# Kernel tuning notes

Measured on AMD Instinct MI355X. Metric: run time of the kernel, lower is better.

The kernel has to match this reference:

```python
import jax, jax.numpy as jnp
import numpy as np

B, N, D, H, DK = 4, 2048, 1024, 16, 64  # batch, seq, model_dim, heads, key_dim (= value_dim)
NEG = -1e9


def setup_inputs() -> dict:
    key = jax.random.key(0)
    ks = jax.random.split(key, 5)
    X = jax.random.normal(ks[0], (B, N, D), dtype=jnp.float32)
    # causal additive mask [N, N]; module slices mask[:N, :M] and adds to logits
    mask = jnp.where(jnp.tril(jnp.ones((N, N), dtype=bool)), 0.0, NEG).astype(jnp.float32)
    s = 1.0 / np.sqrt(D)
    Wq = jax.random.normal(ks[1], (D, H * DK), dtype=jnp.float32) * s
    Wk = jax.random.normal(ks[2], (D, H * DK), dtype=jnp.float32) * s
    Wv = jax.random.normal(ks[3], (D, H * DK), dtype=jnp.float32) * s
    Wo = jax.random.normal(ks[4], (H * DK, D), dtype=jnp.float32) * s
    return {"X": X, "mask": mask, "Wq": Wq, "Wk": Wk, "Wv": Wv, "Wo": Wo}


def reference(X, mask, Wq, Wk, Wv, Wo):
    # Linear projections (bias=False), then split heads: [B,N,H,DK] -> [B,H,N,DK]
    Q = (X @ Wq).reshape(B, N, H, DK).transpose(0, 2, 1, 3)
    K = (X @ Wk).reshape(B, N, H, DK).transpose(0, 2, 1, 3)
    V = (X @ Wv).reshape(B, N, H, DK).transpose(0, 2, 1, 3)
    # full [B,H,N,N] attention logits (module materializes it explicitly)
    att = jnp.einsum('bhnd,bhmd->bhnm', Q, K) / jnp.sqrt(jnp.float32(DK))
    # dropout is in eval mode here -> identity; then additive mask[:N,:M]
    att = att + mask[:N, :N]
    prob = jax.nn.softmax(att, axis=-1)
    values = jnp.einsum('bhnm,bhmd->bhnd', prob, V)
    values_cat = values.transpose(0, 2, 1, 3).reshape(B, N, H * DK)
    return values_cat @ Wo
```

## Files before the change

### kernel.cpp

```cpp
#include <hip/hip_runtime.h>

typedef _Float16 h4  __attribute__((ext_vector_type(4)));
typedef _Float16 v8h __attribute__((ext_vector_type(8)));
typedef float    v4f __attribute__((ext_vector_type(4)));

constexpr int Bn = 4, Nn = 2048, Dn = 1024, Hn = 16, DKn = 64, Mn = 8192;

__device__ __forceinline__ void load_lds16(const _Float16* g, _Float16* l) {
    __builtin_amdgcn_global_load_lds(
        (const __attribute__((address_space(1))) void*)g,
        (__attribute__((address_space(3))) void*)l, 16, 0, 0);
}

__global__ __launch_bounds__(256) void cast_f16(const float* __restrict__ x,
                                                _Float16* __restrict__ y) {
    const int i = blockIdx.x * 256 + threadIdx.x;
    const float4 v = ((const float4*)x)[i];
    h4 o; o[0] = (_Float16)v.x; o[1] = (_Float16)v.y;
    o[2] = (_Float16)v.z; o[3] = (_Float16)v.w;
    ((h4*)y)[i] = o;
}

__global__ __launch_bounds__(256) void castW4(const float* __restrict__ Wq,
                                              const float* __restrict__ Wk,
                                              const float* __restrict__ Wv,
                                              const float* __restrict__ Wo,
                                              _Float16* __restrict__ Wqkv,
                                              _Float16* __restrict__ Wto) {
    __shared__ float tile[32][33];
    const int which = blockIdx.x >> 10, bid = blockIdx.x & 1023;
    const float* W = which == 0 ? Wq : which == 1 ? Wk : which == 2 ? Wv : Wo;
    _Float16* Dst = which < 3 ? (Wqkv + ((size_t)which << 20)) : Wto;
    const int bx = bid & 31, by = bid >> 5;
    const int t = threadIdx.x;
    const int r = t >> 3, c4 = (t & 7) * 4;
    const float4 v = *(const float4*)&W[(size_t)(by * 32 + r) * Dn + bx * 32 + c4];
    tile[r][c4 + 0] = v.x; tile[r][c4 + 1] = v.y;
    tile[r][c4 + 2] = v.z; tile[r][c4 + 3] = v.w;
    __syncthreads();
    h4 o;
    o[0] = (_Float16)tile[c4 + 0][r];
    o[1] = (_Float16)tile[c4 + 1][r];
    o[2] = (_Float16)tile[c4 + 2][r];
    o[3] = (_Float16)tile[c4 + 3][r];
    *(h4*)&Dst[(size_t)(bx * 32 + r) * Dn + by * 32 + c4] = o;
}

#define GEMM_KLOOP(Abase, Bbase)                                                    \
    v4f acc[4][4];                                                                  \
    _Pragma("unroll") for (int i = 0; i < 4; ++i)                                   \
        _Pragma("unroll") for (int j = 0; j < 4; ++j) acc[i][j] = v4f{0,0,0,0};     \
    const int sw8 = (quad ^ (l16 >> 2)) * 8;                                        \
    for (int k0 = 0; k0 < Dn; k0 += 32) {                                           \
        __syncthreads();                                                            \
        _Pragma("unroll") for (int jj = 0; jj < 2; ++jj) {                          \
            const int ci = jj * 256 + w * 64 + lane;                                \
            const int rs = ci >> 2, cs = ci & 3;                                    \
            const int gc = (cs ^ ((rs >> 2) & 3)) * 8;                              \
            load_lds16(Abase + (size_t)rs * Dn + k0 + gc, &As[(jj*256 + w*64) * 8]);\
            load_lds16(Bbase + (size_t)rs * Dn + k0 + gc, &Bs[(jj*256 + w*64) * 8]);\
        }                                                                           \
        __syncthreads();                                                            \
        v8h a[4], b[4];                                                             \
        _Pragma("unroll") for (int i = 0; i < 4; ++i)                               \
            a[i] = *(const v8h*)&As[(wm*64 + i*16 + l16) * 32 + sw8];               \
        _Pragma("unroll") for (int j = 0; j < 4; ++j)                               \
            b[j] = *(const v8h*)&Bs[(wn*64 + j*16 + l16) * 32 + sw8];               \
        _Pragma("unroll") for (int i = 0; i < 4; ++i)                               \
            _Pragma("unroll") for (int j = 0; j < 4; ++j)                           \
                acc[i][j] = __builtin_amdgcn_mfma_f32_16x16x32_f16(a[i], b[j],      \
                                                                   acc[i][j],0,0,0);\
    }

__global__ __launch_bounds__(256) void gemmqkv(const _Float16* __restrict__ A,
                                               const _Float16* __restrict__ Wt,
                                               _Float16* __restrict__ Qo,
                                               _Float16* __restrict__ Ko,
                                               _Float16* __restrict__ Vo)
{
    __shared__ __align__(16) _Float16 As[128 * 32];
    __shared__ __align__(16) _Float16 Bs[128 * 32];
    const int t = threadIdx.x, lane = t & 63, w = t >> 6;
    const int quad = lane >> 4, l16 = lane & 15;
    const int wm = w >> 1, wn = w & 1;
    const int bx = blockIdx.x % 24, by = blockIdx.x / 24;
    const int m0 = by * 128, n0 = bx * 128;
    const _Float16* Abase = A + (size_t)m0 * Dn;
    const _Float16* Bbase = Wt + (size_t)n0 * Dn;

    GEMM_KLOOP(Abase, Bbase)

    const int sec = n0 >> 10;
    if (sec < 2) {
        _Float16* C = sec ? Ko : Qo;
        const float scale = sec ? 1.0f : 0.125f * 1.44269504f;
#pragma unroll
        for (int i = 0; i < 4; ++i) {
            const int mbase = m0 + wm * 64 + i * 16 + quad * 4;
#pragma unroll
            for (int j = 0; j < 4; ++j) {
                const int nl = (n0 + wn * 64 + j * 16 + l16) & 1023;
                const int h = nl >> 6, dk = nl & 63;
#pragma unroll
                for (int r = 0; r < 4; ++r) {
                    const int m = mbase + r, b = m >> 11, nr = m & (Nn - 1);
                    C[((size_t)(b * Hn + h) * Nn + nr) * DKn + dk] = (_Float16)(acc[i][j][r] * scale);
                }
            }
        }
    } else {
#pragma unroll
        for (int i = 0; i < 4; ++i) {
            const int mbase = m0 + wm * 64 + i * 16 + quad * 4;
            const int b = mbase >> 11, nr = mbase & (Nn - 1);
#pragma unroll
            for (int j = 0; j < 4; ++j) {
                const int nl = (n0 + wn * 64 + j * 16 + l16) & 1023;
                const int h = nl >> 6, dk = nl & 63;
                h4 o; o[0] = (_Float16)acc[i][j][0]; o[1] = (_Float16)acc[i][j][1];
                o[2] = (_Float16)acc[i][j][2]; o[3] = (_Float16)acc[i][j][3];
                *(h4*)&Vo[((size_t)(b * Hn + h) * DKn + dk) * Nn + nr] = o;
            }
        }
    }
}

__global__ __launch_bounds__(256) void gemmo(const _Float16* __restrict__ A,
                                             const _Float16* __restrict__ Wt,
                                             float* __restrict__ C)
{
    __shared__ __align__(16) _Float16 As[128 * 32];
    __shared__ __align__(16) _Float16 Bs[128 * 32];
    const int t = threadIdx.x, lane = t & 63, w = t >> 6;
    const int quad = lane >> 4, l16 = lane & 15;
    const int wm = w >> 1, wn = w & 1;
    const int bx = blockIdx.x & 7, by = blockIdx.x >> 3;
    const int m0 = by * 128, n0 = bx * 128;
    const _Float16* Abase = A + (size_t)m0 * Dn;
    const _Float16* Bbase = Wt + (size_t)n0 * Dn;

    GEMM_KLOOP(Abase, Bbase)

#pragma unroll
    for (int i = 0; i < 4; ++i) {
        const int mbase = m0 + wm * 64 + i * 16 + quad * 4;
#pragma unroll
        for (int j = 0; j < 4; ++j) {
            const int n = n0 + wn * 64 + j * 16 + l16;
#pragma unroll
            for (int r = 0; r < 4; ++r)
                C[(size_t)(mbase + r) * Dn + n] = acc[i][j][r];
        }
    }
}

__global__ __launch_bounds__(256) void flashv4(const _Float16* __restrict__ Q,
                                               const _Float16* __restrict__ K,
                                               const _Float16* __restrict__ Vt,
                                               _Float16* __restrict__ O)
{
    __shared__ __align__(16) _Float16 KS[2][64 * 64];
    __shared__ __align__(16) _Float16 VS[2][64 * 64];
    __shared__ __align__(16) _Float16 Ps[4][32][72];

    const int t = threadIdx.x;
    const int lane = t & 63, w = t >> 6;
    const int quad = lane >> 4, l16 = lane & 15;
    const int bh = blockIdx.x & 63;
    const int qtile = 15 - (blockIdx.x >> 6);
    const int b = bh >> 4, h = bh & 15;
    const int qb = qtile * 128 + w * 32;

    const _Float16* Qg = Q  + (size_t)bh * Nn * DKn;
    const _Float16* Kg = K  + (size_t)bh * Nn * DKn;
    const _Float16* Vg = Vt + (size_t)bh * DKn * Nn;

    auto stage = [&](int buf, int kt) {
        const int k0 = kt * 64;
#pragma unroll
        for (int jj = 0; jj < 2; ++jj) {
            const int ci = jj * 256 + w * 64 + lane;
            const int r = ci >> 3, c = ci & 7;
            const int gc = (c ^ (r & 7)) * 8;
            load_lds16(Kg + (size_t)(k0 + r) * DKn + gc, &KS[buf][(jj * 256 + w * 64) * 8]);
            load_lds16(Vg + (size_t)r * Nn + k0 + gc,    &VS[buf][(jj * 256 + w * 64) * 8]);
        }
    };
#define SWZ(arr, r, c) (*(const v8h*)&(arr)[(r) * 64 + (((c) ^ ((r) & 7)) * 8)])

    v8h qf[2][2];
#pragma unroll
    for (int qq = 0; qq < 2; ++qq)
#pragma unroll
        for (int ks = 0; ks < 2; ++ks)
            qf[qq][ks] = *(const v8h*)&Qg[(size_t)(qb + qq * 16 + l16) * DKn + ks * 32 + quad * 8];

    v4f o[2][4];
#pragma unroll
    for (int mq = 0; mq < 2; ++mq)
#pragma unroll
        for (int nt = 0; nt < 4; ++nt) o[mq][nt] = v4f{0.f, 0.f, 0.f, 0.f};
    float lsum[2] = {0.f, 0.f};

    const int nkt = 2 * qtile + 2;
    stage(0, 0);

    for (int kt = 0; kt < nkt; ++kt) {
        const int buf = kt & 1;
        __syncthreads();
        if (kt + 1 < nkt) stage(buf ^ 1, kt + 1);

        const int k0 = kt * 64;
        const _Float16* Ks = KS[buf];
        const _Float16* Vs = VS[buf];

        v4f s[4][2];
#pragma unroll
        for (int kk = 0; kk < 4; ++kk)
#pragma unroll
            for (int qq = 0; qq < 2; ++qq) s[kk][qq] = v4f{0.f, 0.f, 0.f, 0.f};
#pragma unroll
        for (int ks = 0; ks < 2; ++ks)
#pragma unroll
            for (int kk = 0; kk < 4; ++kk) {
                const v8h ak = SWZ(Ks, kk * 16 + l16, ks * 4 + quad);
#pragma unroll
                for (int qq = 0; qq < 2; ++qq)
                    s[kk][qq] = __builtin_amdgcn_mfma_f32_16x16x32_f16(ak, qf[qq][ks], s[kk][qq], 0, 0, 0);
            }

#pragma unroll
        for (int kk = 0; kk < 4; ++kk)
#pragma unroll
            for (int qq = 0; qq < 2; ++qq) {
                const int q = qb + qq * 16 + l16;
                const int key0 = k0 + kk * 16 + quad * 4;
                h4 pk;
#pragma unroll
                for (int r = 0; r < 4; ++r) {
                    const float sv = (key0 + r > q) ? -1e9f : s[kk][qq][r];
                    const float p = exp2f(sv);
                    lsum[qq] += p;
                    pk[r] = (_Float16)p;
                }
                *(h4*)&Ps[w][qq * 16 + l16][kk * 16 + quad * 4] = pk;
            }

#pragma unroll
        for (int ks = 0; ks < 2; ++ks)
#pragma unroll
            for (int mq = 0; mq < 2; ++mq) {
                const v8h a = *(const v8h*)&Ps[w][mq * 16 + l16][ks * 32 + quad * 8];
#pragma unroll
                for (int nt = 0; nt < 4; ++nt) {
                    const v8h bv = SWZ(Vs, nt * 16 + l16, ks * 4 + quad);
                    o[mq][nt] = __builtin_amdgcn_mfma_f32_16x16x32_f16(a, bv, o[mq][nt], 0, 0, 0);
                }
            }
    }
#undef SWZ

    float linv[2];
#pragma unroll
    for (int qq = 0; qq < 2; ++qq) {
        float l = lsum[qq];
        l += __shfl_xor(l, 16);
        l += __shfl_xor(l, 32);
        linv[qq] = 1.0f / l;
    }

    _Float16* Op = O + (size_t)b * Nn * Dn + h * DKn;
#pragma unroll
    for (int mq = 0; mq < 2; ++mq)
#pragma unroll
        for (int r = 0; r < 4; ++r) {
            const float li = __shfl(linv[mq], quad * 4 + r);
            const int qrow = qb + mq * 16 + quad * 4 + r;
#pragma unroll
            for (int nt = 0; nt < 4; ++nt)
                Op[(size_t)qrow * Dn + nt * 16 + l16] = (_Float16)(o[mq][nt][r] * li);
        }
}

extern "C" void kernel_launch(void* const* d_in, const int* in_sizes, int n_in,
                              void* d_out, int out_size, void* d_ws, size_t ws_size,
                              hipStream_t stream)
{
    const float* X  = (const float*)d_in[0];
    const float* Wq = (const float*)d_in[2];
    const float* Wk = (const float*)d_in[3];
    const float* Wv = (const float*)d_in[4];
    const float* Wo = (const float*)d_in[5];

    char* ws = (char*)d_ws;
    _Float16* Xh   = (_Float16*)ws;
    _Float16* Wqkv = (_Float16*)(ws + (16u << 20));
    _Float16* Wto  = Wqkv + (3u << 20);
    _Float16* Qh   = Wto + (1u << 20);
    _Float16* Kh   = Qh + (size_t)Mn * Dn;
    _Float16* Vth  = Kh + (size_t)Mn * Dn;
    _Float16* Ah   = Vth + (size_t)Mn * Dn;

    cast_f16<<<(Mn * Dn / 4) / 256, 256, 0, stream>>>(X, Xh);
    castW4<<<4096, 256, 0, stream>>>(Wq, Wk, Wv, Wo, Wqkv, Wto);
    gemmqkv<<<64 * 24, 256, 0, stream>>>(Xh, Wqkv, Qh, Kh, Vth);
    flashv4<<<1024, 256, 0, stream>>>(Qh, Kh, Vth, Ah);
    gemmo<<<512, 256, 0, stream>>>(Ah, Wto, (float*)d_out);
}
```

Measured before the change: 287.4 us.

## Skip fully-masked key tiles per wave and compute row sums via MFMA

The attention kernel now lets each wave skip key tiles beyond its own causal diagonal, and applies the mask only on the diagonal tile. Row sums of probabilities come from an extra MFMA against a vector of ones, which removes the scalar accumulation and cross-lane shuffles. Probabilities are packed with cvt_pkrtz and stored to a swizzled LDS buffer without padding. In exchange, the K/V double buffering is removed: each tile is loaded synchronously and guarded by two barriers per iteration, so load latency is no longer overlapped with compute.

```diff
diff --git a/kernel.cpp b/kernel.cpp
--- a/kernel.cpp
+++ b/kernel.cpp
@@ -1,8 +1,10 @@
 #include <hip/hip_runtime.h>
 
+typedef __fp16   f2  __attribute__((ext_vector_type(2)));
 typedef _Float16 h4  __attribute__((ext_vector_type(4)));
 typedef _Float16 v8h __attribute__((ext_vector_type(8)));
 typedef float    v4f __attribute__((ext_vector_type(4)));
+struct f2x2 { f2 lo, hi; };
 
 constexpr int Bn = 4, Nn = 2048, Dn = 1024, Hn = 16, DKn = 64, Mn = 8192;
 
@@ -154,14 +156,14 @@
     }
 }
 
-__global__ __launch_bounds__(256) void flashv4(const _Float16* __restrict__ Q,
+__global__ __launch_bounds__(256) void flashv5(const _Float16* __restrict__ Q,
                                                const _Float16* __restrict__ K,
                                                const _Float16* __restrict__ Vt,
                                                _Float16* __restrict__ O)
 {
-    __shared__ __align__(16) _Float16 KS[2][64 * 64];
-    __shared__ __align__(16) _Float16 VS[2][64 * 64];
-    __shared__ __align__(16) _Float16 Ps[4][32][72];
+    __shared__ __align__(16) _Float16 KS[64 * 64];
+    __shared__ __align__(16) _Float16 VS[64 * 64];
+    __shared__ __align__(16) _Float16 Ps[4][32 * 64];
 
     const int t = threadIdx.x;
     const int lane = t & 63, w = t >> 6;
@@ -175,15 +177,15 @@
     const _Float16* Kg = K  + (size_t)bh * Nn * DKn;
     const _Float16* Vg = Vt + (size_t)bh * DKn * Nn;
 
-    auto stage = [&](int buf, int kt) {
+    auto stage = [&](int kt) {
         const int k0 = kt * 64;
 #pragma unroll
         for (int jj = 0; jj < 2; ++jj) {
             const int ci = jj * 256 + w * 64 + lane;
             const int r = ci >> 3, c = ci & 7;
             const int gc = (c ^ (r & 7)) * 8;
-            load_lds16(Kg + (size_t)(k0 + r) * DKn + gc, &KS[buf][(jj * 256 + w * 64) * 8]);
-            load_lds16(Vg + (size_t)r * Nn + k0 + gc,    &VS[buf][(jj * 256 + w * 64) * 8]);
+            load_lds16(Kg + (size_t)(k0 + r) * DKn + gc, &KS[(jj * 256 + w * 64) * 8]);
+            load_lds16(Vg + (size_t)r * Nn + k0 + gc,    &VS[(jj * 256 + w * 64) * 8]);
         }
     };
 #define SWZ(arr, r, c) (*(const v8h*)&(arr)[(r) * 64 + (((c) ^ ((r) & 7)) * 8)])
@@ -195,86 +197,83 @@
         for (int ks = 0; ks < 2; ++ks)
             qf[qq][ks] = *(const v8h*)&Qg[(size_t)(qb + qq * 16 + l16) * DKn + ks * 32 + quad * 8];
 
+    v8h ones;
+#pragma unroll
+    for (int i = 0; i < 8; ++i) ones[i] = (_Float16)1.0f;
+
     v4f o[2][4];
 #pragma unroll
     for (int mq = 0; mq < 2; ++mq)
 #pragma unroll
         for (int nt = 0; nt < 4; ++nt) o[mq][nt] = v4f{0.f, 0.f, 0.f, 0.f};
-    float lsum[2] = {0.f, 0.f};
-
-    const int nkt = 2 * qtile + 2;
-    stage(0, 0);
-
-    for (int kt = 0; kt < nkt; ++kt) {
-        const int buf = kt & 1;
+    v4f ol[2] = {v4f{0.f, 0.f, 0.f, 0.f}, v4f{0.f, 0.f, 0.f, 0.f}};
+
+    const int NKT  = 2 * qtile + 2;
+    const int diag = 2 * qtile + (w >> 1);
+
+    for (int kt = 0; kt < NKT; ++kt) {
+        stage(kt);
         __syncthreads();
-        if (kt + 1 < nkt) stage(buf ^ 1, kt + 1);
-
-        const int k0 = kt * 64;
-        const _Float16* Ks = KS[buf];
-        const _Float16* Vs = VS[buf];
-
-        v4f s[4][2];
-#pragma unroll
-        for (int kk = 0; kk < 4; ++kk)
-#pragma unroll
-            for (int qq = 0; qq < 2; ++qq) s[kk][qq] = v4f{0.f, 0.f, 0.f, 0.f};
-#pragma unroll
-        for (int ks = 0; ks < 2; ++ks)
-#pragma unroll
-            for (int kk = 0; kk < 4; ++kk) {
-                const v8h ak = SWZ(Ks, kk * 16 + l16, ks * 4 + quad);
-#pragma unroll
-                for (int qq = 0; qq < 2; ++qq)
-                    s[kk][qq] = __builtin_amdgcn_mfma_f32_16x16x32_f16(ak, qf[qq][ks], s[kk][qq], 0, 0, 0);
-            }
-
-#pragma unroll
-        for (int kk = 0; kk < 4; ++kk)
-#pragma unroll
-            for (int qq = 0; qq < 2; ++qq) {
-                const int q = qb + qq * 16 + l16;
-                const int key0 = k0 + kk * 16 + quad * 4;
-                h4 pk;
-#pragma unroll
-                for (int r = 0; r < 4; ++r) {
-                    const float sv = (key0 + r > q) ? -1e9f : s[kk][qq][r];
-                    const float p = exp2f(sv);
-                    lsum[qq] += p;
-                    pk[r] = (_Float16)p;
+        if (kt <= diag) {
+            const int k0 = kt * 64;
+            auto ptile = [&](bool domask) {
+#pragma unroll
+                for (int kk = 0; kk < 4; ++kk) {
+                    v4f s0 = v4f{0.f, 0.f, 0.f, 0.f}, s1 = v4f{0.f, 0.f, 0.f, 0.f};
+#pragma unroll
+                    for (int ks = 0; ks < 2; ++ks) {
+                        const v8h ak = SWZ(KS, kk * 16 + l16, ks * 4 + quad);
+                        s0 = __builtin_amdgcn_mfma_f32_16x16x32_f16(ak, qf[0][ks], s0, 0, 0, 0);
+                        s1 = __builtin_amdgcn_mfma_f32_16x16x32_f16(ak, qf[1][ks], s1, 0, 0, 0);
+                    }
+                    const int key0 = k0 + kk * 16 + quad * 4;
+#pragma unroll
+                    for (int qq = 0; qq < 2; ++qq) {
+                        const v4f sv = qq ? s1 : s0;
+                        const int q = qb + qq * 16 + l16;
+                        float p[4];
+#pragma unroll
+                        for (int r = 0; r < 4; ++r) {
+                            float x = sv[r];
+                            if (domask) x = (key0 + r > q) ? -1e9f : x;
+                            p[r] = exp2f(x);
+                        }
+                        f2x2 pkr;
+                        pkr.lo = __builtin_amdgcn_cvt_pkrtz(p[0], p[1]);
+                        pkr.hi = __builtin_amdgcn_cvt_pkrtz(p[2], p[3]);
+                        const h4 pk = __builtin_bit_cast(h4, pkr);
+                        const int prow = qq * 16 + l16;
+                        const int pch  = kk * 2 + (quad >> 1);
+                        *(h4*)&Ps[w][prow * 64 + ((pch ^ (prow & 7)) * 8 + (quad & 1) * 4)] = pk;
+                    }
                 }
-                *(h4*)&Ps[w][qq * 16 + l16][kk * 16 + quad * 4] = pk;
-            }
-
-#pragma unroll
-        for (int ks = 0; ks < 2; ++ks)
-#pragma unroll
-            for (int mq = 0; mq < 2; ++mq) {
-                const v8h a = *(const v8h*)&Ps[w][mq * 16 + l16][ks * 32 + quad * 8];
-#pragma unroll
-                for (int nt = 0; nt < 4; ++nt) {
-                    const v8h bv = SWZ(Vs, nt * 16 + l16, ks * 4 + quad);
-                    o[mq][nt] = __builtin_amdgcn_mfma_f32_16x16x32_f16(a, bv, o[mq][nt], 0, 0, 0);
-                }
-            }
+#pragma unroll
+                for (int ks = 0; ks < 2; ++ks)
+#pragma unroll
+                    for (int mq = 0; mq < 2; ++mq) {
+                        const int arow = mq * 16 + l16;
+                        const int ach  = ks * 4 + quad;
+                        const v8h a = *(const v8h*)&Ps[w][arow * 64 + ((ach ^ (arow & 7)) * 8)];
+#pragma unroll
+                        for (int nt = 0; nt < 4; ++nt) {
+                            const v8h bvv = SWZ(VS, nt * 16 + l16, ks * 4 + quad);
+                            o[mq][nt] = __builtin_amdgcn_mfma_f32_16x16x32_f16(a, bvv, o[mq][nt], 0, 0, 0);
+                        }
+                        ol[mq] = __builtin_amdgcn_mfma_f32_16x16x32_f16(a, ones, ol[mq], 0, 0, 0);
+                    }
+            };
+            if (kt == diag) ptile(true); else ptile(false);
+        }
+        __syncthreads();
     }
 #undef SWZ
 
-    float linv[2];
-#pragma unroll
-    for (int qq = 0; qq < 2; ++qq) {
-        float l = lsum[qq];
-        l += __shfl_xor(l, 16);
-        l += __shfl_xor(l, 32);
-        linv[qq] = 1.0f / l;
-    }
-
     _Float16* Op = O + (size_t)b * Nn * Dn + h * DKn;
 #pragma unroll
     for (int mq = 0; mq < 2; ++mq)
 #pragma unroll
         for (int r = 0; r < 4; ++r) {
-            const float li = __shfl(linv[mq], quad * 4 + r);
+            const float li = 1.0f / ol[mq][r];
             const int qrow = qb + mq * 16 + quad * 4 + r;
 #pragma unroll
             for (int nt = 0; nt < 4; ++nt)
@@ -304,6 +303,6 @@
     cast_f16<<<(Mn * Dn / 4) / 256, 256, 0, stream>>>(X, Xh);
     castW4<<<4096, 256, 0, stream>>>(Wq, Wk, Wv, Wo, Wqkv, Wto);
     gemmqkv<<<64 * 24, 256, 0, stream>>>(Xh, Wqkv, Qh, Kh, Vth);
-    flashv4<<<1024, 256, 0, stream>>>(Qh, Kh, Vth, Ah);
+    flashv5<<<1024, 256, 0, stream>>>(Qh, Kh, Vth, Ah);
     gemmo<<<512, 256, 0, stream>>>(Ah, Wto, (float*)d_out);
 }
```

Result: faster. 270.8 us (-5.8%).
